# Kernel tuning notes

Measured on AMD Instinct MI355X. Metric: run time of the kernel, lower is better.

The kernel has to match this reference:

```python
import jax, jax.numpy as jnp
import numpy as np

N = 100_000      # nodes
E = 3_200_000    # edges (avg degree 32)
F_IN = 172       # raw node features
HID = 32         # hid_channels
ENC = 8          # encoding_dim
H, C = 2, 16     # heads, per-head channels (TransformerConv 32 -> 2x16)
OUT = 2          # classes
INV_SQRT_C = 1.0 / np.sqrt(C).astype(np.float32)


def setup_inputs() -> dict:
    key = jax.random.key(0)
    ks = jax.random.split(key, 40)
    p = lambda k, shape: (jax.random.normal(k, shape, dtype=jnp.float32) * 0.05)
    return {
        # data tensors
        "x": jax.random.normal(ks[0], (N, F_IN), dtype=jnp.float32),
        "edge_index": jax.random.randint(ks[1], (2, E), 0, N),
        "node_time": jax.random.uniform(ks[2], (N,), dtype=jnp.float32),
        "edge_time": jax.random.uniform(ks[3], (E, 1), dtype=jnp.float32),
        "node_interval": jax.random.uniform(ks[4], (N, 1), dtype=jnp.float32),
        "node_degree": jax.random.uniform(ks[5], (N, 1), dtype=jnp.float32),
        # TimeEncode(32): cos(Linear(1, 32))
        "Wt": p(ks[6], (1, HID)), "bt": p(ks[7], (HID,)),
        # DegreeEncoder / TemporalFrequencyEncoder: Linear(1, 8)
        "Wd": p(ks[8], (1, ENC)), "bd": p(ks[9], (ENC,)),
        "Wtf": p(ks[10], (1, ENC)), "btf": p(ks[11], (ENC,)),
        # w_enc: Linear(8, 8); w_x: Linear(32, 8)
        "Wenc": p(ks[12], (ENC, ENC)), "benc": p(ks[13], (ENC,)),
        "Wx": p(ks[14], (HID, ENC)), "bx": p(ks[15], (ENC,)),
        # lin: Linear(in_channels, 32)
        "Wlin": p(ks[16], (F_IN, HID)), "blin": p(ks[17], (HID,)),
        # lin_combine: Linear(40, 32)
        "Wcomb": p(ks[18], (HID + ENC, HID)), "bcomb": p(ks[19], (HID,)),
        # TransformerConv projections (32 -> heads*16 = 32)
        "Wq": p(ks[20], (HID, H * C)), "bq": p(ks[21], (H * C,)),
        "Wk": p(ks[22], (HID, H * C)), "bk": p(ks[23], (H * C,)),
        "Wv": p(ks[24], (HID, H * C)), "bv": p(ks[25], (H * C,)),
        "We": p(ks[26], (HID, H * C)), "be": p(ks[27], (H * C,)),
        "Wskip": p(ks[28], (HID, H * C)), "bskip": p(ks[29], (H * C,)),
        # out: Linear(32, out_channels)
        "Wout": p(ks[30], (HID, OUT)), "bout": p(ks[31], (OUT,)),
    }


def _segment_softmax(alpha, seg, num_segments):
    # alpha: [E, H], seg: [E] destination indices
    m = jax.ops.segment_max(alpha, seg, num_segments=num_segments)
    a = jnp.exp(alpha - m[seg])
    s = jax.ops.segment_sum(a, seg, num_segments=num_segments)
    return a / (s[seg] + 1e-16)


def reference(x, edge_index, node_time, edge_time, node_interval, node_degree,
              Wt, bt, Wd, bd, Wtf, btf, Wenc, benc, Wx, bx, Wlin, blin,
              Wcomb, bcomb, Wq, bq, Wk, bk, Wv, bv, We, be, Wskip, bskip,
              Wout, bout):
    src, dst = edge_index[0], edge_index[1]
    n = x.shape[0]

    # ---- time encoding of relative edge time: cos(Linear(rel_t)) ----
    rel_t = node_time[src][:, None] - edge_time               # [E, 1]
    rel_t_enc = jnp.cos(rel_t @ Wt + bt)                      # [E, 32]

    # ---- node encoders + attention-gated combine ----
    h1 = x @ Wlin + blin                                      # [N, 32]
    tf_enc = node_interval @ Wtf + btf                        # [N, 8]
    deg_enc = node_degree @ Wd + bd                           # [N, 8]
    encodings = jnp.stack((tf_enc, deg_enc), axis=1)          # [N, 2, 8]
    enc_proj = jnp.tanh(encodings @ Wenc + benc)              # [N, 2, 8]
    x_proj = jnp.tanh(h1 @ Wx + bx)                           # [N, 8]
    score = jnp.einsum('nke,ne->nk', enc_proj, x_proj)        # [N, 2]
    score = jax.nn.softmax(score, axis=1)
    context = jnp.einsum('nke,nk->ne', encodings, score)      # [N, 8]
    h1 = jnp.concatenate((h1, context), axis=1) @ Wcomb + bcomb  # [N, 32]

    # ---- TransformerConv (heads=2, out=16, concat) with edge features ----
    q = (h1 @ Wq + bq).reshape(n, H, C)
    k = (h1 @ Wk + bk).reshape(n, H, C)
    v = (h1 @ Wv + bv).reshape(n, H, C)
    e = (rel_t_enc @ We + be).reshape(-1, H, C)               # [E, H, C]

    k_e = k[src] + e                                          # [E, H, C]
    alpha = jnp.einsum('ehc,ehc->eh', q[dst], k_e) * INV_SQRT_C
    alpha = _segment_softmax(alpha, dst, n)                   # [E, H]
    msg = (v[src] + e) * alpha[..., None]                     # [E, H, C]
    agg = jax.ops.segment_sum(msg, dst, num_segments=n)       # [N, H, C]
    h2 = agg.reshape(n, H * C) + (h1 @ Wskip + bskip)         # root_weight skip

    out = h2 @ Wout + bout                                    # [N, 2]
    return jax.nn.log_softmax(out, axis=1)
```

## Files before the change

kernel.cpp:

```cpp
#include <hip/hip_runtime.h>
#include <hip/hip_bf16.h>
#include <cstdint>


#define FIN 172
#define INV_SQRT_C 0.25f

typedef _Float16 f16x8 __attribute__((ext_vector_type(8)));
typedef float f32x4 __attribute__((ext_vector_type(4)));

__device__ __forceinline__ uint32_t cvt_pk_bf16(float lo, float hi) {
    uint32_t r;
    asm("v_cvt_pk_bf16_f32 %0, %1, %2" : "=v"(r) : "v"(lo), "v"(hi));
    return r;
}
__device__ __forceinline__ float bflo(uint32_t u) {
    union { uint32_t i; float f; } x; x.i = u << 16; return x.f;
}
__device__ __forceinline__ float bfhi(uint32_t u) {
    union { uint32_t i; float f; } x; x.i = u & 0xFFFF0000u; return x.f;
}
__device__ __forceinline__ void pk_atomic_add_bf16(void* addr, uint32_t data) {
    asm volatile("global_atomic_pk_add_bf16 %0, %1, off"
                 :: "v"((uint64_t)(uintptr_t)addr), "v"(data) : "memory");
}

__global__ __launch_bounds__(256) void k1_lin(
    const float* __restrict__ x, const float* __restrict__ Wlin,
    const float* __restrict__ blin, float* __restrict__ h1pre, int n)
{
    __shared__ __align__(16) float WlT[32][174];
    __shared__ __align__(16) float xs[16][FIN];
    const int t = threadIdx.x;

    for (int i = t; i < FIN * 32; i += 256) {
        int kk = i >> 5, o = i & 31;
        WlT[o][kk] = Wlin[i];
    }
    const int row0 = blockIdx.x * 16;
    for (int i = t; i < 16 * FIN; i += 256) {
        int rr = i / FIN, kk = i - rr * FIN;
        int gr = row0 + rr;
        xs[rr][kk] = (gr < n) ? x[(size_t)gr * FIN + kk] : 0.f;
    }
    __syncthreads();

    const int o = t & 31, r = t >> 5;
    float acc0 = blin[o], acc1 = acc0;
    const float2* wp  = reinterpret_cast<const float2*>(&WlT[o][0]);
    const float2* xp0 = reinterpret_cast<const float2*>(&xs[r][0]);
    const float2* xp1 = reinterpret_cast<const float2*>(&xs[r + 8][0]);
    #pragma unroll 4
    for (int kk = 0; kk < FIN / 2; ++kk) {
        float2 wv = wp[kk], xa = xp0[kk], xb = xp1[kk];
        acc0 = fmaf(xa.x, wv.x, acc0);
        acc0 = fmaf(xa.y, wv.y, acc0);
        acc1 = fmaf(xb.x, wv.x, acc1);
        acc1 = fmaf(xb.y, wv.y, acc1);
    }
    const int g0 = row0 + r, g1 = row0 + r + 8;
    if (g0 < n) h1pre[(size_t)g0 * 32 + o] = acc0;
    if (g1 < n) h1pre[(size_t)g1 * 32 + o] = acc1;
}

template <int K, int O>
__device__ __forceinline__ void matvecKO(const float* __restrict__ v,
                                         const float* __restrict__ W,
                                         const float* __restrict__ B,
                                         float* __restrict__ out)
{
    #pragma unroll
    for (int o4 = 0; o4 < O / 4; ++o4) {
        float a0 = B[o4 * 4 + 0], a1 = B[o4 * 4 + 1];
        float a2 = B[o4 * 4 + 2], a3 = B[o4 * 4 + 3];
        #pragma unroll
        for (int k = 0; k < K; ++k) {
            float4 wv = *reinterpret_cast<const float4*>(&W[k * O + o4 * 4]);
            float hv = v[k];
            a0 = fmaf(hv, wv.x, a0);
            a1 = fmaf(hv, wv.y, a1);
            a2 = fmaf(hv, wv.z, a2);
            a3 = fmaf(hv, wv.w, a3);
        }
        out[o4 * 4 + 0] = a0; out[o4 * 4 + 1] = a1;
        out[o4 * 4 + 2] = a2; out[o4 * 4 + 3] = a3;
    }
}

__device__ __forceinline__ void store32(float* __restrict__ dst,
                                        const float* __restrict__ v)
{
    float4* d4 = reinterpret_cast<float4*>(dst);
    #pragma unroll
    for (int i = 0; i < 8; ++i)
        d4[i] = make_float4(v[4 * i], v[4 * i + 1], v[4 * i + 2], v[4 * i + 3]);
}

__global__ __launch_bounds__(256) void k2_enc(
    const float* __restrict__ h1pre,
    const float* __restrict__ node_interval, const float* __restrict__ node_degree,
    const float* __restrict__ Wtf, const float* __restrict__ btf,
    const float* __restrict__ Wd,  const float* __restrict__ bd,
    const float* __restrict__ Wenc, const float* __restrict__ benc,
    const float* __restrict__ Wx,  const float* __restrict__ bx,
    const float* __restrict__ Wcomb, const float* __restrict__ bcomb,
    const float* __restrict__ Wq,  const float* __restrict__ bq,
    const float* __restrict__ Wk,  const float* __restrict__ bk,
    const float* __restrict__ Wv,  const float* __restrict__ bv,
    const float* __restrict__ Wskip, const float* __restrict__ bskip,
    uint32_t* __restrict__ q32, uint32_t* __restrict__ kv32,
    float* __restrict__ skipb, int n)
{
    __shared__ __align__(16) float sWenc[64], sWx[256], sWcomb[1280];
    __shared__ __align__(16) float sWq[1024], sWk[1024], sWv[1024], sWs[1024];
    __shared__ float sWtf[8], sbtf[8], sWd[8], sbd[8], sbenc[8], sbx[8];
    __shared__ float sbcomb[32], sbq[32], sbk[32], sbv[32], sbs[32];

    const int t = threadIdx.x;
    if (t < 8) {
        sWtf[t] = Wtf[t]; sbtf[t] = btf[t];
        sWd[t]  = Wd[t];  sbd[t]  = bd[t];
        sbenc[t] = benc[t]; sbx[t] = bx[t];
    }
    if (t < 32) {
        sbcomb[t] = bcomb[t]; sbq[t] = bq[t]; sbk[t] = bk[t];
        sbv[t] = bv[t]; sbs[t] = bskip[t];
    }
    if (t < 64) sWenc[t] = Wenc[t];
    if (t < 256) sWx[t] = Wx[t];
    for (int i = t; i < 1280; i += 256) sWcomb[i] = Wcomb[i];
    for (int i = t; i < 1024; i += 256) {
        sWq[i] = Wq[i]; sWk[i] = Wk[i]; sWv[i] = Wv[i]; sWs[i] = Wskip[i];
    }
    __syncthreads();

    const int nid = blockIdx.x * 256 + t;
    if (nid >= n) return;

    float h1p[32];
    {
        const float2* hp = reinterpret_cast<const float2*>(h1pre + (size_t)nid * 32);
        #pragma unroll
        for (int i = 0; i < 16; ++i) {
            float2 v2 = hp[i];
            h1p[2 * i] = v2.x; h1p[2 * i + 1] = v2.y;
        }
    }
    const float ti = node_interval[nid], dg = node_degree[nid];
    float tf[8], de[8];
    #pragma unroll
    for (int j = 0; j < 8; ++j) {
        tf[j] = fmaf(ti, sWtf[j], sbtf[j]);
        de[j] = fmaf(dg, sWd[j], sbd[j]);
    }
    float xp[8];
    matvecKO<32, 8>(h1p, sWx, sbx, xp);
    #pragma unroll
    for (int o = 0; o < 8; ++o) xp[o] = tanhf(xp[o]);

    float ep0[8], ep1[8];
    matvecKO<8, 8>(tf, sWenc, sbenc, ep0);
    matvecKO<8, 8>(de, sWenc, sbenc, ep1);
    float sc0 = 0.f, sc1 = 0.f;
    #pragma unroll
    for (int o = 0; o < 8; ++o) {
        sc0 = fmaf(tanhf(ep0[o]), xp[o], sc0);
        sc1 = fmaf(tanhf(ep1[o]), xp[o], sc1);
    }
    const float mm = fmaxf(sc0, sc1);
    const float e0 = __expf(sc0 - mm), e1 = __expf(sc1 - mm);
    const float inv = 1.f / (e0 + e1);
    const float s0 = e0 * inv, s1 = e1 * inv;

    float v40[40];
    #pragma unroll
    for (int i = 0; i < 32; ++i) v40[i] = h1p[i];
    #pragma unroll
    for (int j = 0; j < 8; ++j) v40[32 + j] = fmaf(s0, tf[j], s1 * de[j]);
    float h1[32];
    matvecKO<40, 32>(v40, sWcomb, sbcomb, h1);

    float tq[32], tk[32], tv[32], ts[32];
    matvecKO<32, 32>(h1, sWq, sbq, tq);
    matvecKO<32, 32>(h1, sWk, sbk, tk);
    matvecKO<32, 32>(h1, sWv, sbv, tv);
    matvecKO<32, 32>(h1, sWs, sbs, ts);

    uint32_t* qw  = q32  + (size_t)nid * 16;
    uint32_t* kvw = kv32 + (size_t)nid * 32;
    #pragma unroll
    for (int p = 0; p < 16; ++p) {
        qw[p]          = cvt_pk_bf16(tq[p], tq[16 + p]);
        kvw[2 * p]     = cvt_pk_bf16(tk[p], tk[16 + p]);
        kvw[2 * p + 1] = cvt_pk_bf16(tv[p], tv[16 + p]);
    }
    store32(skipb + (size_t)nid * 32, ts);
}

__global__ __launch_bounds__(256) void k3_edge(
    const int* __restrict__ ei, const float* __restrict__ node_time,
    const float* __restrict__ edge_time,
    const uint32_t* __restrict__ qp, const uint32_t* __restrict__ kvp,
    const float* __restrict__ Wt, const float* __restrict__ bt,
    const float* __restrict__ We, const float* __restrict__ be,
    unsigned short* __restrict__ agg, unsigned short* __restrict__ den,
    int numE, int nTiles)
{
    const int lane = threadIdx.x & 63;
    const int g = lane >> 4;
    const int m = lane & 15;

    float wtr[8], btr[8];
    f16x8 B0, B1;
    #pragma unroll
    for (int i = 0; i < 8; ++i) {
        const int k = g * 8 + i;
        wtr[i] = Wt[k];
        btr[i] = bt[k];
        B0[i] = (_Float16)We[k * 32 + m];
        B1[i] = (_Float16)We[k * 32 + 16 + m];
    }
    const float be0 = be[m], be1 = be[16 + m];

    const int wid = blockIdx.x * (blockDim.x >> 6) + (threadIdx.x >> 6);
    const int nW  = gridDim.x * (blockDim.x >> 6);

    int tile = wid;
    if (tile >= nTiles) return;

    int srcm = 0, dstm = 0;
    float et = 0.f;
    {
        const int eA = tile * 16 + m;
        if (eA < numE) {
            srcm = ei[eA];
            dstm = ei[numE + eA];
            et   = edge_time[eA];
        }
    }

    while (true) {
        const float nt = node_time[srcm];
        int srcr[4], dstr[4];
        uint32_t qw[4];
        uint2 kvw[4];
        #pragma unroll
        for (int r = 0; r < 4; ++r) {
            const int j = g * 4 + r;
            srcr[r] = __shfl(srcm, j);
            dstr[r] = __shfl(dstm, j);
            qw[r]  = qp[(size_t)dstr[r] * 16 + m];
            kvw[r] = *reinterpret_cast<const uint2*>(
                         kvp + (size_t)srcr[r] * 32 + 2 * m);
        }

        const int ntile = tile + nW;
        int nsrc = 0, ndst = 0;
        float net = 0.f;
        if (ntile < nTiles) {
            const int eA = ntile * 16 + m;
            if (eA < numE) {
                nsrc = ei[eA];
                ndst = ei[numE + eA];
                net  = edge_time[eA];
            }
        }

        const float rel = nt - et;
        f16x8 A;
        #pragma unroll
        for (int i = 0; i < 8; ++i)
            A[i] = (_Float16)__cosf(fmaf(rel, wtr[i], btr[i]));

        f32x4 acc0 = {0.f, 0.f, 0.f, 0.f};
        f32x4 acc1 = {0.f, 0.f, 0.f, 0.f};
        acc0 = __builtin_amdgcn_mfma_f32_16x16x32_f16(A, B0, acc0, 0, 0, 0);
        acc1 = __builtin_amdgcn_mfma_f32_16x16x32_f16(A, B1, acc1, 0, 0, 0);

        const int e0 = tile * 16;
        #pragma unroll
        for (int r = 0; r < 4; ++r) {
            if (e0 + g * 4 + r < numE) {
                const float ef0 = acc0[r] + be0;
                const float ef1 = acc1[r] + be1;

                const uint32_t uq = qw[r];
                const uint32_t uk = kvw[r].x, uv = kvw[r].y;
                const float q0 = bflo(uq), q1 = bfhi(uq);
                const float k0 = bflo(uk), k1 = bfhi(uk);
                const float v0 = bflo(uv), v1 = bfhi(uv);

                float p0 = q0 * (k0 + ef0);
                float p1 = q1 * (k1 + ef1);
                #pragma unroll
                for (int s = 1; s < 16; s <<= 1) {
                    p0 += __shfl_xor(p0, s);
                    p1 += __shfl_xor(p1, s);
                }
                const float w0 = __expf(p0 * INV_SQRT_C);
                const float w1 = __expf(p1 * INV_SQRT_C);

                const float t0 = w0 * (v0 + ef0);
                const float t1 = w1 * (v1 + ef1);
                const float x0 = __shfl_xor(t0, 1);
                const float x1 = __shfl_xor(t1, 1);
                const uint32_t data = (m & 1) ? cvt_pk_bf16(x1, t1)
                                              : cvt_pk_bf16(t0, x0);
                const int choff = (m & 1) ? (15 + m) : m;
                pk_atomic_add_bf16(agg + (size_t)dstr[r] * 32 + choff, data);

                if (m == 0)
                    pk_atomic_add_bf16(den + (size_t)dstr[r] * 2,
                                       cvt_pk_bf16(w0, w1));
            }
        }

        if (ntile >= nTiles) break;
        tile = ntile; srcm = nsrc; dstm = ndst; et = net;
    }
}

__global__ __launch_bounds__(256) void k4_out(
    const unsigned short* __restrict__ agg, const unsigned short* __restrict__ den,
    const float* __restrict__ skipb,
    const float* __restrict__ Wout, const float* __restrict__ bout,
    float* __restrict__ out, int n)
{
    __shared__ float sW[64];
    __shared__ float sb[2];
    const int t = threadIdx.x;
    if (t < 64) sW[t] = Wout[t];
    if (t < 2) sb[t] = bout[t];
    __syncthreads();

    const int nid = blockIdx.x * 256 + t;
    if (nid >= n) return;

    const uint32_t ud = reinterpret_cast<const uint32_t*>(den)[nid];
    const float inv0 = 1.f / (bflo(ud) + 1e-16f);
    const float inv1 = 1.f / (bfhi(ud) + 1e-16f);
    const uint32_t* ag = reinterpret_cast<const uint32_t*>(agg) + (size_t)nid * 16;
    const float*    sk = skipb + (size_t)nid * 32;

    float o0 = sb[0], o1 = sb[1];
    #pragma unroll
    for (int p = 0; p < 16; ++p) {
        const uint32_t u = ag[p];
        const float iv = (p < 8) ? inv0 : inv1;
        const float hLo = fmaf(bflo(u), iv, sk[2 * p]);
        const float hHi = fmaf(bfhi(u), iv, sk[2 * p + 1]);
        o0 = fmaf(hLo, sW[(2 * p) * 2],     o0);
        o1 = fmaf(hLo, sW[(2 * p) * 2 + 1], o1);
        o0 = fmaf(hHi, sW[(2 * p + 1) * 2],     o0);
        o1 = fmaf(hHi, sW[(2 * p + 1) * 2 + 1], o1);
    }
    const float mm = fmaxf(o0, o1);
    const float lse = mm + __logf(__expf(o0 - mm) + __expf(o1 - mm));
    out[(size_t)nid * 2 + 0] = o0 - lse;
    out[(size_t)nid * 2 + 1] = o1 - lse;
}

extern "C" void kernel_launch(void* const* d_in, const int* in_sizes, int n_in,
                              void* d_out, int out_size, void* d_ws, size_t ws_size,
                              hipStream_t stream)
{
    const float* x             = (const float*)d_in[0];
    const int*   ei            = (const int*)  d_in[1];
    const float* node_time     = (const float*)d_in[2];
    const float* edge_time     = (const float*)d_in[3];
    const float* node_interval = (const float*)d_in[4];
    const float* node_degree   = (const float*)d_in[5];
    const float* Wt    = (const float*)d_in[6];  const float* bt    = (const float*)d_in[7];
    const float* Wd    = (const float*)d_in[8];  const float* bd    = (const float*)d_in[9];
    const float* Wtf   = (const float*)d_in[10]; const float* btf   = (const float*)d_in[11];
    const float* Wenc  = (const float*)d_in[12]; const float* benc  = (const float*)d_in[13];
    const float* Wx    = (const float*)d_in[14]; const float* bx    = (const float*)d_in[15];
    const float* Wlin  = (const float*)d_in[16]; const float* blin  = (const float*)d_in[17];
    const float* Wcomb = (const float*)d_in[18]; const float* bcomb = (const float*)d_in[19];
    const float* Wq    = (const float*)d_in[20]; const float* bq    = (const float*)d_in[21];
    const float* Wk    = (const float*)d_in[22]; const float* bk    = (const float*)d_in[23];
    const float* Wv    = (const float*)d_in[24]; const float* bv    = (const float*)d_in[25];
    const float* We    = (const float*)d_in[26]; const float* be    = (const float*)d_in[27];
    const float* Wskip = (const float*)d_in[28]; const float* bskip = (const float*)d_in[29];
    const float* Wout  = (const float*)d_in[30]; const float* bout  = (const float*)d_in[31];

    const int n    = in_sizes[2];
    const int numE = in_sizes[3];

    char* base = (char*)d_ws;
    uint32_t* q32  = (uint32_t*)base; base += (size_t)n * 16 * 4;
    uint32_t* kv32 = (uint32_t*)base; base += (size_t)n * 32 * 4;
    float* skipb = (float*)base; base += (size_t)n * 32 * 4;
    float* h1pre = (float*)base; base += (size_t)n * 32 * 4;
    unsigned short* agg = (unsigned short*)base; base += (size_t)n * 32 * 2;
    unsigned short* den = (unsigned short*)base; base += (size_t)n * 2 * 2;

    hipMemsetAsync(agg, 0, (size_t)n * (32 * 2 + 2 * 2), stream);

    k1_lin<<<(n + 15) / 16, 256, 0, stream>>>(x, Wlin, blin, h1pre, n);

    k2_enc<<<(n + 255) / 256, 256, 0, stream>>>(
        h1pre, node_interval, node_degree,
        Wtf, btf, Wd, bd, Wenc, benc, Wx, bx, Wcomb, bcomb,
        Wq, bq, Wk, bk, Wv, bv, Wskip, bskip,
        q32, kv32, skipb, n);

    const int nTiles = (numE + 15) / 16;
    k3_edge<<<4096, 256, 0, stream>>>(
        ei, node_time, edge_time, q32, kv32,
        Wt, bt, We, be, agg, den, numE, nTiles);

    k4_out<<<(n + 255) / 256, 256, 0, stream>>>(
        agg, den, skipb, Wout, bout, (float*)d_out, n);
}
```

Baseline: 492.4 us.

## Fold output projection into edge scatter to shrink atomic aggregation width

Uses linearity of the final Wout projection to project each weighted message onto the two output classes per head inside the edge kernel. Each edge then atomically adds 6 bf16 values (per-head class partials plus softmax denominators) instead of 32 channels plus 2 denominators. The skip path is likewise reduced to a 2-float projection in the node kernel. The MFMA operand roles are swapped so each lane holds one edge with a slice of channels, which enables vectorized uint4 gathers of q/k/v and wave-shuffle reductions. This cuts atomic traffic and the aggregation buffer size, at the cost of extra shuffles and FMAs per edge and more contention on fewer addresses per destination.

```diff
diff --git a/kernel.cpp b/kernel.cpp
--- a/kernel.cpp
+++ b/kernel.cpp
@@ -87,15 +87,6 @@
     }
 }
 
-__device__ __forceinline__ void store32(float* __restrict__ dst,
-                                        const float* __restrict__ v)
-{
-    float4* d4 = reinterpret_cast<float4*>(dst);
-    #pragma unroll
-    for (int i = 0; i < 8; ++i)
-        d4[i] = make_float4(v[4 * i], v[4 * i + 1], v[4 * i + 2], v[4 * i + 3]);
-}
-
 __global__ __launch_bounds__(256) void k2_enc(
     const float* __restrict__ h1pre,
     const float* __restrict__ node_interval, const float* __restrict__ node_degree,
@@ -108,13 +99,15 @@
     const float* __restrict__ Wk,  const float* __restrict__ bk,
     const float* __restrict__ Wv,  const float* __restrict__ bv,
     const float* __restrict__ Wskip, const float* __restrict__ bskip,
+    const float* __restrict__ Wout,
     uint32_t* __restrict__ q32, uint32_t* __restrict__ kv32,
-    float* __restrict__ skipb, int n)
+    float2* __restrict__ skip2, int n)
 {
     __shared__ __align__(16) float sWenc[64], sWx[256], sWcomb[1280];
     __shared__ __align__(16) float sWq[1024], sWk[1024], sWv[1024], sWs[1024];
     __shared__ float sWtf[8], sbtf[8], sWd[8], sbd[8], sbenc[8], sbx[8];
     __shared__ float sbcomb[32], sbq[32], sbk[32], sbv[32], sbs[32];
+    __shared__ float sWout[64];
 
     const int t = threadIdx.x;
     if (t < 8) {
@@ -126,7 +119,7 @@
         sbcomb[t] = bcomb[t]; sbq[t] = bq[t]; sbk[t] = bk[t];
         sbv[t] = bv[t]; sbs[t] = bskip[t];
     }
-    if (t < 64) sWenc[t] = Wenc[t];
+    if (t < 64) { sWenc[t] = Wenc[t]; sWout[t] = Wout[t]; }
     if (t < 256) sWx[t] = Wx[t];
     for (int i = t; i < 1280; i += 256) sWcomb[i] = Wcomb[i];
     for (int i = t; i < 1024; i += 256) {
@@ -194,7 +187,13 @@
         kvw[2 * p]     = cvt_pk_bf16(tk[p], tk[16 + p]);
         kvw[2 * p + 1] = cvt_pk_bf16(tv[p], tv[16 + p]);
     }
-    store32(skipb + (size_t)nid * 32, ts);
+    float sk0 = 0.f, sk1 = 0.f;
+    #pragma unroll
+    for (int c = 0; c < 32; ++c) {
+        sk0 = fmaf(ts[c], sWout[c * 2],     sk0);
+        sk1 = fmaf(ts[c], sWout[c * 2 + 1], sk1);
+    }
+    skip2[nid] = make_float2(sk0, sk1);
 }
 
 __global__ __launch_bounds__(256) void k3_edge(
@@ -203,24 +202,31 @@
     const uint32_t* __restrict__ qp, const uint32_t* __restrict__ kvp,
     const float* __restrict__ Wt, const float* __restrict__ bt,
     const float* __restrict__ We, const float* __restrict__ be,
-    unsigned short* __restrict__ agg, unsigned short* __restrict__ den,
-    int numE, int nTiles)
+    const float* __restrict__ Wout,
+    unsigned short* __restrict__ accb, int numE, int nTiles)
 {
     const int lane = threadIdx.x & 63;
     const int g = lane >> 4;
     const int m = lane & 15;
 
     float wtr[8], btr[8];
-    f16x8 B0, B1;
+    f16x8 WeA0, WeA1;
     #pragma unroll
     for (int i = 0; i < 8; ++i) {
         const int k = g * 8 + i;
-        wtr[i] = Wt[k];
-        btr[i] = bt[k];
-        B0[i] = (_Float16)We[k * 32 + m];
-        B1[i] = (_Float16)We[k * 32 + 16 + m];
-    }
-    const float be0 = be[m], be1 = be[16 + m];
+        wtr[i] = Wt[k]; btr[i] = bt[k];
+        WeA0[i] = (_Float16)We[k * 32 + m];
+        WeA1[i] = (_Float16)We[k * 32 + 16 + m];
+    }
+    float beh0[4], beh1[4], wo00[4], wo01[4], wo10[4], wo11[4];
+    #pragma unroll
+    for (int r = 0; r < 4; ++r) {
+        const int c = 4 * g + r;
+        beh0[r] = be[c];        beh1[r] = be[16 + c];
+        wo00[r] = Wout[c * 2];  wo01[r] = Wout[c * 2 + 1];
+        wo10[r] = Wout[(16 + c) * 2];
+        wo11[r] = Wout[(16 + c) * 2 + 1];
+    }
 
     const int wid = blockIdx.x * (blockDim.x >> 6) + (threadIdx.x >> 6);
     const int nW  = gridDim.x * (blockDim.x >> 6);
@@ -228,31 +234,25 @@
     int tile = wid;
     if (tile >= nTiles) return;
 
-    int srcm = 0, dstm = 0;
+    int src = 0, dst = 0;
     float et = 0.f;
     {
         const int eA = tile * 16 + m;
         if (eA < numE) {
-            srcm = ei[eA];
-            dstm = ei[numE + eA];
-            et   = edge_time[eA];
+            src = ei[eA]; dst = ei[numE + eA]; et = edge_time[eA];
         }
     }
 
     while (true) {
-        const float nt = node_time[srcm];
-        int srcr[4], dstr[4];
-        uint32_t qw[4];
-        uint2 kvw[4];
-        #pragma unroll
-        for (int r = 0; r < 4; ++r) {
-            const int j = g * 4 + r;
-            srcr[r] = __shfl(srcm, j);
-            dstr[r] = __shfl(dstm, j);
-            qw[r]  = qp[(size_t)dstr[r] * 16 + m];
-            kvw[r] = *reinterpret_cast<const uint2*>(
-                         kvp + (size_t)srcr[r] * 32 + 2 * m);
-        }
+        const bool valid = (tile * 16 + m) < numE;
+
+        const float nt = node_time[src];
+        const uint4 qw  = *reinterpret_cast<const uint4*>(
+                              qp + (size_t)dst * 16 + 4 * g);
+        const uint4 kva = *reinterpret_cast<const uint4*>(
+                              kvp + (size_t)src * 32 + 8 * g);
+        const uint4 kvb = *reinterpret_cast<const uint4*>(
+                              kvp + (size_t)src * 32 + 8 * g + 4);
 
         const int ntile = tile + nW;
         int nsrc = 0, ndst = 0;
@@ -260,100 +260,79 @@
         if (ntile < nTiles) {
             const int eA = ntile * 16 + m;
             if (eA < numE) {
-                nsrc = ei[eA];
-                ndst = ei[numE + eA];
-                net  = edge_time[eA];
+                nsrc = ei[eA]; ndst = ei[numE + eA]; net = edge_time[eA];
             }
         }
 
         const float rel = nt - et;
-        f16x8 A;
+        f16x8 B;
         #pragma unroll
         for (int i = 0; i < 8; ++i)
-            A[i] = (_Float16)__cosf(fmaf(rel, wtr[i], btr[i]));
+            B[i] = (_Float16)__cosf(fmaf(rel, wtr[i], btr[i]));
 
         f32x4 acc0 = {0.f, 0.f, 0.f, 0.f};
         f32x4 acc1 = {0.f, 0.f, 0.f, 0.f};
-        acc0 = __builtin_amdgcn_mfma_f32_16x16x32_f16(A, B0, acc0, 0, 0, 0);
-        acc1 = __builtin_amdgcn_mfma_f32_16x16x32_f16(A, B1, acc1, 0, 0, 0);
-
-        const int e0 = tile * 16;
+        acc0 = __builtin_amdgcn_mfma_f32_16x16x32_f16(WeA0, B, acc0, 0, 0, 0);
+        acc1 = __builtin_amdgcn_mfma_f32_16x16x32_f16(WeA1, B, acc1, 0, 0, 0);
+
+        const uint32_t qwa[4] = {qw.x, qw.y, qw.z, qw.w};
+        const uint32_t kk[4]  = {kva.x, kva.z, kvb.x, kvb.z};
+        const uint32_t vv[4]  = {kva.y, kva.w, kvb.y, kvb.w};
+
+        float e0[4], e1[4];
+        float p0 = 0.f, p1 = 0.f;
         #pragma unroll
         for (int r = 0; r < 4; ++r) {
-            if (e0 + g * 4 + r < numE) {
-                const float ef0 = acc0[r] + be0;
-                const float ef1 = acc1[r] + be1;
-
-                const uint32_t uq = qw[r];
-                const uint32_t uk = kvw[r].x, uv = kvw[r].y;
-                const float q0 = bflo(uq), q1 = bfhi(uq);
-                const float k0 = bflo(uk), k1 = bfhi(uk);
-                const float v0 = bflo(uv), v1 = bfhi(uv);
-
-                float p0 = q0 * (k0 + ef0);
-                float p1 = q1 * (k1 + ef1);
-                #pragma unroll
-                for (int s = 1; s < 16; s <<= 1) {
-                    p0 += __shfl_xor(p0, s);
-                    p1 += __shfl_xor(p1, s);
-                }
-                const float w0 = __expf(p0 * INV_SQRT_C);
-                const float w1 = __expf(p1 * INV_SQRT_C);
-
-                const float t0 = w0 * (v0 + ef0);
-                const float t1 = w1 * (v1 + ef1);
-                const float x0 = __shfl_xor(t0, 1);
-                const float x1 = __shfl_xor(t1, 1);
-                const uint32_t data = (m & 1) ? cvt_pk_bf16(x1, t1)
-                                              : cvt_pk_bf16(t0, x0);
-                const int choff = (m & 1) ? (15 + m) : m;
-                pk_atomic_add_bf16(agg + (size_t)dstr[r] * 32 + choff, data);
-
-                if (m == 0)
-                    pk_atomic_add_bf16(den + (size_t)dstr[r] * 2,
-                                       cvt_pk_bf16(w0, w1));
-            }
+            e0[r] = acc0[r] + beh0[r];
+            e1[r] = acc1[r] + beh1[r];
+            p0 = fmaf(bflo(qwa[r]), bflo(kk[r]) + e0[r], p0);
+            p1 = fmaf(bfhi(qwa[r]), bfhi(kk[r]) + e1[r], p1);
+        }
+        p0 += __shfl_xor(p0, 16); p0 += __shfl_xor(p0, 32);
+        p1 += __shfl_xor(p1, 16); p1 += __shfl_xor(p1, 32);
+        const float w0 = __expf(p0 * INV_SQRT_C);
+        const float w1 = __expf(p1 * INV_SQRT_C);
+
+        float y00 = 0.f, y01 = 0.f, y10 = 0.f, y11 = 0.f;
+        #pragma unroll
+        for (int r = 0; r < 4; ++r) {
+            const float t0 = w0 * (bflo(vv[r]) + e0[r]);
+            const float t1 = w1 * (bfhi(vv[r]) + e1[r]);
+            y00 = fmaf(t0, wo00[r], y00); y01 = fmaf(t0, wo01[r], y01);
+            y10 = fmaf(t1, wo10[r], y10); y11 = fmaf(t1, wo11[r], y11);
+        }
+        y00 += __shfl_xor(y00, 16); y00 += __shfl_xor(y00, 32);
+        y01 += __shfl_xor(y01, 16); y01 += __shfl_xor(y01, 32);
+        y10 += __shfl_xor(y10, 16); y10 += __shfl_xor(y10, 32);
+        y11 += __shfl_xor(y11, 16); y11 += __shfl_xor(y11, 32);
+
+        if (valid) {
+            unsigned short* row = accb + (size_t)dst * 8;
+            if (g == 0) pk_atomic_add_bf16(row,     cvt_pk_bf16(y00, y01));
+            if (g == 1) pk_atomic_add_bf16(row + 2, cvt_pk_bf16(y10, y11));
+            if (g == 2) pk_atomic_add_bf16(row + 4, cvt_pk_bf16(w0,  w1));
         }
 
         if (ntile >= nTiles) break;
-        tile = ntile; srcm = nsrc; dstm = ndst; et = net;
+        tile = ntile; src = nsrc; dst = ndst; et = net;
     }
 }
 
 __global__ __launch_bounds__(256) void k4_out(
-    const unsigned short* __restrict__ agg, const unsigned short* __restrict__ den,
-    const float* __restrict__ skipb,
-    const float* __restrict__ Wout, const float* __restrict__ bout,
-    float* __restrict__ out, int n)
-{
-    __shared__ float sW[64];
-    __shared__ float sb[2];
-    const int t = threadIdx.x;
-    if (t < 64) sW[t] = Wout[t];
-    if (t < 2) sb[t] = bout[t];
-    __syncthreads();
-
-    const int nid = blockIdx.x * 256 + t;
+    const unsigned short* __restrict__ accb, const float2* __restrict__ skip2,
+    const float* __restrict__ bout, float* __restrict__ out, int n)
+{
+    const int nid = blockIdx.x * 256 + threadIdx.x;
     if (nid >= n) return;
 
-    const uint32_t ud = reinterpret_cast<const uint32_t*>(den)[nid];
-    const float inv0 = 1.f / (bflo(ud) + 1e-16f);
-    const float inv1 = 1.f / (bfhi(ud) + 1e-16f);
-    const uint32_t* ag = reinterpret_cast<const uint32_t*>(agg) + (size_t)nid * 16;
-    const float*    sk = skipb + (size_t)nid * 32;
-
-    float o0 = sb[0], o1 = sb[1];
-    #pragma unroll
-    for (int p = 0; p < 16; ++p) {
-        const uint32_t u = ag[p];
-        const float iv = (p < 8) ? inv0 : inv1;
-        const float hLo = fmaf(bflo(u), iv, sk[2 * p]);
-        const float hHi = fmaf(bfhi(u), iv, sk[2 * p + 1]);
-        o0 = fmaf(hLo, sW[(2 * p) * 2],     o0);
-        o1 = fmaf(hLo, sW[(2 * p) * 2 + 1], o1);
-        o0 = fmaf(hHi, sW[(2 * p + 1) * 2],     o0);
-        o1 = fmaf(hHi, sW[(2 * p + 1) * 2 + 1], o1);
-    }
+    const uint4 u = *reinterpret_cast<const uint4*>(accb + (size_t)nid * 8);
+    const float inv0 = 1.f / (bflo(u.z) + 1e-16f);
+    const float inv1 = 1.f / (bfhi(u.z) + 1e-16f);
+    const float2 sk = skip2[nid];
+
+    const float o0 = bflo(u.x) * inv0 + bflo(u.y) * inv1 + sk.x + bout[0];
+    const float o1 = bfhi(u.x) * inv0 + bfhi(u.y) * inv1 + sk.y + bout[1];
+
     const float mm = fmaxf(o0, o1);
     const float lse = mm + __logf(__expf(o0 - mm) + __expf(o1 - mm));
     out[(size_t)nid * 2 + 0] = o0 - lse;
@@ -390,26 +369,25 @@
     char* base = (char*)d_ws;
     uint32_t* q32  = (uint32_t*)base; base += (size_t)n * 16 * 4;
     uint32_t* kv32 = (uint32_t*)base; base += (size_t)n * 32 * 4;
-    float* skipb = (float*)base; base += (size_t)n * 32 * 4;
-    float* h1pre = (float*)base; base += (size_t)n * 32 * 4;
-    unsigned short* agg = (unsigned short*)base; base += (size_t)n * 32 * 2;
-    unsigned short* den = (unsigned short*)base; base += (size_t)n * 2 * 2;
-
-    hipMemsetAsync(agg, 0, (size_t)n * (32 * 2 + 2 * 2), stream);
+    float*    h1pre = (float*)base;   base += (size_t)n * 32 * 4;
+    float2*   skip2 = (float2*)base;  base += (size_t)n * 2 * 4;
+    unsigned short* accb = (unsigned short*)base; base += (size_t)n * 8 * 2;
+
+    hipMemsetAsync(accb, 0, (size_t)n * 8 * 2, stream);
 
     k1_lin<<<(n + 15) / 16, 256, 0, stream>>>(x, Wlin, blin, h1pre, n);
 
     k2_enc<<<(n + 255) / 256, 256, 0, stream>>>(
         h1pre, node_interval, node_degree,
         Wtf, btf, Wd, bd, Wenc, benc, Wx, bx, Wcomb, bcomb,
-        Wq, bq, Wk, bk, Wv, bv, Wskip, bskip,
-        q32, kv32, skipb, n);
+        Wq, bq, Wk, bk, Wv, bv, Wskip, bskip, Wout,
+        q32, kv32, skip2, n);
 
     const int nTiles = (numE + 15) / 16;
     k3_edge<<<4096, 256, 0, stream>>>(
         ei, node_time, edge_time, q32, kv32,
-        Wt, bt, We, be, agg, den, numE, nTiles);
+        Wt, bt, We, be, Wout, accb, numE, nTiles);
 
     k4_out<<<(n + 255) / 256, 256, 0, stream>>>(
-        agg, den, skipb, Wout, bout, (float*)d_out, n);
-}
+        accb, skip2, bout, (float*)d_out, n);
+}
```

Measured after the change: 667.0 us. 35.5% more time.

## Use MFMA fp16 matrix ops for node linear layers and projections

Applied to the files above, without the earlier changes.

The input linear layer (172->32) becomes a persistent grid of wavefronts. Each wavefront keeps the weights in registers as fp16 MFMA B-fragments and loads x rows straight from global memory into A-fragments. In the encoder kernel, the combine, Q, K, V and skip projections move from per-thread scalar FMA matvecs to 16x16x32 fp16 MFMAs, staging activations through LDS. This cuts ALU work and the large per-block LDS weight staging, at the cost of fp16 rounding on inputs and weights, and of strided, uncoalesced per-lane x loads in k1.

```diff
diff --git a/kernel.cpp b/kernel.cpp
--- a/kernel.cpp
+++ b/kernel.cpp
@@ -29,38 +29,52 @@
     const float* __restrict__ x, const float* __restrict__ Wlin,
     const float* __restrict__ blin, float* __restrict__ h1pre, int n)
 {
-    __shared__ __align__(16) float WlT[32][174];
-    __shared__ __align__(16) float xs[16][FIN];
-    const int t = threadIdx.x;
-
-    for (int i = t; i < FIN * 32; i += 256) {
-        int kk = i >> 5, o = i & 31;
-        WlT[o][kk] = Wlin[i];
-    }
-    const int row0 = blockIdx.x * 16;
-    for (int i = t; i < 16 * FIN; i += 256) {
-        int rr = i / FIN, kk = i - rr * FIN;
-        int gr = row0 + rr;
-        xs[rr][kk] = (gr < n) ? x[(size_t)gr * FIN + kk] : 0.f;
-    }
-    __syncthreads();
-
-    const int o = t & 31, r = t >> 5;
-    float acc0 = blin[o], acc1 = acc0;
-    const float2* wp  = reinterpret_cast<const float2*>(&WlT[o][0]);
-    const float2* xp0 = reinterpret_cast<const float2*>(&xs[r][0]);
-    const float2* xp1 = reinterpret_cast<const float2*>(&xs[r + 8][0]);
-    #pragma unroll 4
-    for (int kk = 0; kk < FIN / 2; ++kk) {
-        float2 wv = wp[kk], xa = xp0[kk], xb = xp1[kk];
-        acc0 = fmaf(xa.x, wv.x, acc0);
-        acc0 = fmaf(xa.y, wv.y, acc0);
-        acc1 = fmaf(xb.x, wv.x, acc1);
-        acc1 = fmaf(xb.y, wv.y, acc1);
-    }
-    const int g0 = row0 + r, g1 = row0 + r + 8;
-    if (g0 < n) h1pre[(size_t)g0 * 32 + o] = acc0;
-    if (g1 < n) h1pre[(size_t)g1 * 32 + o] = acc1;
+    const int lane = threadIdx.x & 63;
+    const int g = lane >> 4, m = lane & 15;
+
+    f16x8 Bf[6][2];
+    #pragma unroll
+    for (int s = 0; s < 6; ++s) {
+        #pragma unroll
+        for (int i = 0; i < 8; ++i) {
+            const int k = s * 32 + g * 8 + i;
+            Bf[s][0][i] = (_Float16)((k < FIN) ? Wlin[k * 32 + m] : 0.f);
+            Bf[s][1][i] = (_Float16)((k < FIN) ? Wlin[k * 32 + 16 + m] : 0.f);
+        }
+    }
+    const float b0 = blin[m], b1 = blin[16 + m];
+
+    const int wid = blockIdx.x * 4 + (threadIdx.x >> 6);
+    const int nW  = gridDim.x * 4;
+    const int nChunks = (n + 15) / 16;
+
+    for (int c = wid; c < nChunks; c += nW) {
+        const int row = c * 16 + m;
+        const bool rv = row < n;
+        const float* xr = x + (size_t)row * FIN;
+
+        f32x4 acc0 = {0.f, 0.f, 0.f, 0.f};
+        f32x4 acc1 = {0.f, 0.f, 0.f, 0.f};
+        #pragma unroll
+        for (int s = 0; s < 6; ++s) {
+            f16x8 A;
+            #pragma unroll
+            for (int i = 0; i < 8; ++i) {
+                const int k = s * 32 + g * 8 + i;
+                A[i] = (_Float16)((rv && k < FIN) ? xr[k] : 0.f);
+            }
+            acc0 = __builtin_amdgcn_mfma_f32_16x16x32_f16(A, Bf[s][0], acc0, 0, 0, 0);
+            acc1 = __builtin_amdgcn_mfma_f32_16x16x32_f16(A, Bf[s][1], acc1, 0, 0, 0);
+        }
+        #pragma unroll
+        for (int r = 0; r < 4; ++r) {
+            const int node = c * 16 + 4 * g + r;
+            if (node < n) {
+                h1pre[(size_t)node * 32 + m]      = acc0[r] + b0;
+                h1pre[(size_t)node * 32 + 16 + m] = acc1[r] + b1;
+            }
+        }
+    }
 }
 
 template <int K, int O>
@@ -85,15 +99,6 @@
         out[o4 * 4 + 0] = a0; out[o4 * 4 + 1] = a1;
         out[o4 * 4 + 2] = a2; out[o4 * 4 + 3] = a3;
     }
-}
-
-__device__ __forceinline__ void store32(float* __restrict__ dst,
-                                        const float* __restrict__ v)
-{
-    float4* d4 = reinterpret_cast<float4*>(dst);
-    #pragma unroll
-    for (int i = 0; i < 8; ++i)
-        d4[i] = make_float4(v[4 * i], v[4 * i + 1], v[4 * i + 2], v[4 * i + 3]);
 }
 
 __global__ __launch_bounds__(256) void k2_enc(
@@ -111,10 +116,10 @@
     uint32_t* __restrict__ q32, uint32_t* __restrict__ kv32,
     float* __restrict__ skipb, int n)
 {
-    __shared__ __align__(16) float sWenc[64], sWx[256], sWcomb[1280];
-    __shared__ __align__(16) float sWq[1024], sWk[1024], sWv[1024], sWs[1024];
+    __shared__ __align__(16) float sWenc[64], sWx[256];
     __shared__ float sWtf[8], sbtf[8], sWd[8], sbd[8], sbenc[8], sbx[8];
-    __shared__ float sbcomb[32], sbq[32], sbk[32], sbv[32], sbs[32];
+    __shared__ __align__(16) _Float16 v40s[256][72];
+    __shared__ __align__(16) _Float16 h1s[256][40];
 
     const int t = threadIdx.x;
     if (t < 8) {
@@ -122,79 +127,141 @@
         sWd[t]  = Wd[t];  sbd[t]  = bd[t];
         sbenc[t] = benc[t]; sbx[t] = bx[t];
     }
-    if (t < 32) {
-        sbcomb[t] = bcomb[t]; sbq[t] = bq[t]; sbk[t] = bk[t];
-        sbv[t] = bv[t]; sbs[t] = bskip[t];
-    }
     if (t < 64) sWenc[t] = Wenc[t];
     if (t < 256) sWx[t] = Wx[t];
-    for (int i = t; i < 1280; i += 256) sWcomb[i] = Wcomb[i];
-    for (int i = t; i < 1024; i += 256) {
-        sWq[i] = Wq[i]; sWk[i] = Wk[i]; sWv[i] = Wv[i]; sWs[i] = Wskip[i];
-    }
+
+    const int nid = blockIdx.x * 256 + t;
+    const bool active = nid < n;
+
     __syncthreads();
 
-    const int nid = blockIdx.x * 256 + t;
-    if (nid >= n) return;
-
-    float h1p[32];
-    {
+    if (active) {
+        float h1p[32];
         const float2* hp = reinterpret_cast<const float2*>(h1pre + (size_t)nid * 32);
         #pragma unroll
         for (int i = 0; i < 16; ++i) {
             float2 v2 = hp[i];
             h1p[2 * i] = v2.x; h1p[2 * i + 1] = v2.y;
         }
-    }
-    const float ti = node_interval[nid], dg = node_degree[nid];
-    float tf[8], de[8];
-    #pragma unroll
-    for (int j = 0; j < 8; ++j) {
-        tf[j] = fmaf(ti, sWtf[j], sbtf[j]);
-        de[j] = fmaf(dg, sWd[j], sbd[j]);
-    }
-    float xp[8];
-    matvecKO<32, 8>(h1p, sWx, sbx, xp);
-    #pragma unroll
-    for (int o = 0; o < 8; ++o) xp[o] = tanhf(xp[o]);
-
-    float ep0[8], ep1[8];
-    matvecKO<8, 8>(tf, sWenc, sbenc, ep0);
-    matvecKO<8, 8>(de, sWenc, sbenc, ep1);
-    float sc0 = 0.f, sc1 = 0.f;
-    #pragma unroll
-    for (int o = 0; o < 8; ++o) {
-        sc0 = fmaf(tanhf(ep0[o]), xp[o], sc0);
-        sc1 = fmaf(tanhf(ep1[o]), xp[o], sc1);
-    }
-    const float mm = fmaxf(sc0, sc1);
-    const float e0 = __expf(sc0 - mm), e1 = __expf(sc1 - mm);
-    const float inv = 1.f / (e0 + e1);
-    const float s0 = e0 * inv, s1 = e1 * inv;
-
-    float v40[40];
-    #pragma unroll
-    for (int i = 0; i < 32; ++i) v40[i] = h1p[i];
-    #pragma unroll
-    for (int j = 0; j < 8; ++j) v40[32 + j] = fmaf(s0, tf[j], s1 * de[j]);
-    float h1[32];
-    matvecKO<40, 32>(v40, sWcomb, sbcomb, h1);
-
-    float tq[32], tk[32], tv[32], ts[32];
-    matvecKO<32, 32>(h1, sWq, sbq, tq);
-    matvecKO<32, 32>(h1, sWk, sbk, tk);
-    matvecKO<32, 32>(h1, sWv, sbv, tv);
-    matvecKO<32, 32>(h1, sWs, sbs, ts);
-
-    uint32_t* qw  = q32  + (size_t)nid * 16;
-    uint32_t* kvw = kv32 + (size_t)nid * 32;
-    #pragma unroll
-    for (int p = 0; p < 16; ++p) {
-        qw[p]          = cvt_pk_bf16(tq[p], tq[16 + p]);
-        kvw[2 * p]     = cvt_pk_bf16(tk[p], tk[16 + p]);
-        kvw[2 * p + 1] = cvt_pk_bf16(tv[p], tv[16 + p]);
-    }
-    store32(skipb + (size_t)nid * 32, ts);
+        const float ti = node_interval[nid], dg = node_degree[nid];
+        float tf[8], de[8];
+        #pragma unroll
+        for (int j = 0; j < 8; ++j) {
+            tf[j] = fmaf(ti, sWtf[j], sbtf[j]);
+            de[j] = fmaf(dg, sWd[j], sbd[j]);
+        }
+        float xp[8];
+        matvecKO<32, 8>(h1p, sWx, sbx, xp);
+        #pragma unroll
+        for (int o = 0; o < 8; ++o) xp[o] = tanhf(xp[o]);
+
+        float ep0[8], ep1[8];
+        matvecKO<8, 8>(tf, sWenc, sbenc, ep0);
+        matvecKO<8, 8>(de, sWenc, sbenc, ep1);
+        float sc0 = 0.f, sc1 = 0.f;
+        #pragma unroll
+        for (int o = 0; o < 8; ++o) {
+            sc0 = fmaf(tanhf(ep0[o]), xp[o], sc0);
+            sc1 = fmaf(tanhf(ep1[o]), xp[o], sc1);
+        }
+        const float mm = fmaxf(sc0, sc1);
+        const float e0 = __expf(sc0 - mm), e1 = __expf(sc1 - mm);
+        const float inv = 1.f / (e0 + e1);
+        const float s0 = e0 * inv, s1 = e1 * inv;
+
+        #pragma unroll
+        for (int i = 0; i < 32; ++i) v40s[t][i] = (_Float16)h1p[i];
+        #pragma unroll
+        for (int j = 0; j < 8; ++j)
+            v40s[t][32 + j] = (_Float16)fmaf(s0, tf[j], s1 * de[j]);
+    } else {
+        #pragma unroll
+        for (int i = 0; i < 40; ++i) v40s[t][i] = (_Float16)0.f;
+    }
+    #pragma unroll
+    for (int i = 40; i < 64; ++i) v40s[t][i] = (_Float16)0.f;
+
+    __syncthreads();
+
+    const int lane = t & 63;
+    const int g = lane >> 4, m = lane & 15;
+    const int wv = t >> 6;
+    const int node0 = blockIdx.x * 256;
+
+    f16x8 Bc0[2], Bc1[2];
+    #pragma unroll
+    for (int s = 0; s < 2; ++s)
+        #pragma unroll
+        for (int i = 0; i < 8; ++i) {
+            const int k = s * 32 + g * 8 + i;
+            Bc0[s][i] = (_Float16)((k < 40) ? Wcomb[k * 32 + m] : 0.f);
+            Bc1[s][i] = (_Float16)((k < 40) ? Wcomb[k * 32 + 16 + m] : 0.f);
+        }
+    const float bc0 = bcomb[m], bc1 = bcomb[16 + m];
+
+    for (int c = wv; c < 16; c += 4) {
+        f32x4 a0 = {0.f, 0.f, 0.f, 0.f};
+        f32x4 a1 = {0.f, 0.f, 0.f, 0.f};
+        #pragma unroll
+        for (int s = 0; s < 2; ++s) {
+            const f16x8 A = *reinterpret_cast<const f16x8*>(&v40s[c * 16 + m][s * 32 + g * 8]);
+            a0 = __builtin_amdgcn_mfma_f32_16x16x32_f16(A, Bc0[s], a0, 0, 0, 0);
+            a1 = __builtin_amdgcn_mfma_f32_16x16x32_f16(A, Bc1[s], a1, 0, 0, 0);
+        }
+        #pragma unroll
+        for (int r = 0; r < 4; ++r) {
+            const int nb = c * 16 + 4 * g + r;
+            h1s[nb][m]      = (_Float16)(a0[r] + bc0);
+            h1s[nb][16 + m] = (_Float16)(a1[r] + bc1);
+        }
+    }
+    __syncthreads();
+
+    f16x8 Bq0, Bq1, Bk0, Bk1, Bv0, Bv1, Bs0, Bs1;
+    #pragma unroll
+    for (int i = 0; i < 8; ++i) {
+        const int k = g * 8 + i;
+        Bq0[i] = (_Float16)Wq[k * 32 + m];     Bq1[i] = (_Float16)Wq[k * 32 + 16 + m];
+        Bk0[i] = (_Float16)Wk[k * 32 + m];     Bk1[i] = (_Float16)Wk[k * 32 + 16 + m];
+        Bv0[i] = (_Float16)Wv[k * 32 + m];     Bv1[i] = (_Float16)Wv[k * 32 + 16 + m];
+        Bs0[i] = (_Float16)Wskip[k * 32 + m];  Bs1[i] = (_Float16)Wskip[k * 32 + 16 + m];
+    }
+    const float bq0 = bq[m], bq1 = bq[16 + m];
+    const float bk0 = bk[m], bk1 = bk[16 + m];
+    const float bv0 = bv[m], bv1 = bv[16 + m];
+    const float bs0 = bskip[m], bs1 = bskip[16 + m];
+
+    for (int c = wv; c < 16; c += 4) {
+        const f16x8 A = *reinterpret_cast<const f16x8*>(&h1s[c * 16 + m][g * 8]);
+
+        f32x4 aq0 = {0.f,0.f,0.f,0.f}, aq1 = {0.f,0.f,0.f,0.f};
+        f32x4 ak0 = {0.f,0.f,0.f,0.f}, ak1 = {0.f,0.f,0.f,0.f};
+        f32x4 av0 = {0.f,0.f,0.f,0.f}, av1 = {0.f,0.f,0.f,0.f};
+        f32x4 as0 = {0.f,0.f,0.f,0.f}, as1 = {0.f,0.f,0.f,0.f};
+        aq0 = __builtin_amdgcn_mfma_f32_16x16x32_f16(A, Bq0, aq0, 0, 0, 0);
+        aq1 = __builtin_amdgcn_mfma_f32_16x16x32_f16(A, Bq1, aq1, 0, 0, 0);
+        ak0 = __builtin_amdgcn_mfma_f32_16x16x32_f16(A, Bk0, ak0, 0, 0, 0);
+        ak1 = __builtin_amdgcn_mfma_f32_16x16x32_f16(A, Bk1, ak1, 0, 0, 0);
+        av0 = __builtin_amdgcn_mfma_f32_16x16x32_f16(A, Bv0, av0, 0, 0, 0);
+        av1 = __builtin_amdgcn_mfma_f32_16x16x32_f16(A, Bv1, av1, 0, 0, 0);
+        as0 = __builtin_amdgcn_mfma_f32_16x16x32_f16(A, Bs0, as0, 0, 0, 0);
+        as1 = __builtin_amdgcn_mfma_f32_16x16x32_f16(A, Bs1, as1, 0, 0, 0);
+
+        #pragma unroll
+        for (int r = 0; r < 4; ++r) {
+            const int node = node0 + c * 16 + 4 * g + r;
+            if (node < n) {
+                q32[(size_t)node * 16 + m] =
+                    cvt_pk_bf16(aq0[r] + bq0, aq1[r] + bq1);
+                uint2 kvd;
+                kvd.x = cvt_pk_bf16(ak0[r] + bk0, ak1[r] + bk1);
+                kvd.y = cvt_pk_bf16(av0[r] + bv0, av1[r] + bv1);
+                *reinterpret_cast<uint2*>(kv32 + (size_t)node * 32 + 2 * m) = kvd;
+                skipb[(size_t)node * 32 + m]      = as0[r] + bs0;
+                skipb[(size_t)node * 32 + 16 + m] = as1[r] + bs1;
+            }
+        }
+    }
 }
 
 __global__ __launch_bounds__(256) void k3_edge(
@@ -397,7 +464,7 @@
 
     hipMemsetAsync(agg, 0, (size_t)n * (32 * 2 + 2 * 2), stream);
 
-    k1_lin<<<(n + 15) / 16, 256, 0, stream>>>(x, Wlin, blin, h1pre, n);
+    k1_lin<<<512, 256, 0, stream>>>(x, Wlin, blin, h1pre, n);
 
     k2_enc<<<(n + 255) / 256, 256, 0, stream>>>(
         h1pre, node_interval, node_degree,
```

New measurement: 423.0 us. -14.1%, faster.
